# Kernel tuning notes

Measured on AMD Instinct MI355X. Metric: run time of the kernel, lower is better.

Reference implementation:

```python
import jax, jax.numpy as jnp
import numpy as np

EPS = 1e-08
ROUTING_ITERS = 3

def squash(s, axis=-1):
    norm = jnp.linalg.norm(s, axis=axis, keepdims=True)
    return norm / (1.0 + norm ** 2 + EPS) * s

def setup_inputs() -> dict:
    key = jax.random.key(0)
    k1, k2, k3 = jax.random.split(key, 3)
    B, R, C, O, I = 512, 640, 10, 16, 8
    x = jax.random.normal(k1, (B, R, I), dtype=jnp.float32)
    W = jax.random.normal(k2, (R, C, O, I), dtype=jnp.float32) * 0.01
    bias = jax.random.uniform(k3, (1, 1, C, O), dtype=jnp.float32) * 0.01
    return {"x": x, "W": W, "bias": bias}

def reference(x, W, bias):
    # u_hat[b,r,c,o] = sum_i W[r,c,o,i] * x[b,r,i]
    u_hat = jnp.einsum('rcoi,bri->brco', W, x)  # [B,R,C,O]
    u_hat_d = jax.lax.stop_gradient(u_hat)
    B, R, C, _ = u_hat.shape
    b_ij = jnp.zeros((B, R, C, 1), dtype=u_hat.dtype)
    v_j = None
    for itr in range(ROUTING_ITERS):
        c_ij = jax.nn.softmax(b_ij, axis=2)               # softmax over capsules
        s_j = jnp.sum(c_ij * u_hat_d, axis=1, keepdims=True) + bias  # [B,1,C,O]
        v_j = squash(s_j, axis=-1)
        if itr < ROUTING_ITERS - 1:
            a_ij = jnp.sum(u_hat * v_j, axis=-1, keepdims=True)  # agreement, non-detached
            b_ij = b_ij + a_ij
    return jnp.squeeze(v_j, axis=1)  # [B,C,O]
```

## Files before the change

### kernel.cpp

```cpp
#include <hip/hip_runtime.h>
#include <math.h>

#define BB 512
#define RR 640
#define CC 10
#define OO 16
#define CO 160
#define II 8
#define S_FLOATS (BB*CO)

#define ZCH (RR*CO)
#define LSTR 165
#define VSTR 164

#define CG_NRG 16
#define CG_RPW 10

#define FB_NRG 32
#define FB_RPW 5

#define CNT_INTS (96*16)

using f16x8 = __attribute__((ext_vector_type(8))) _Float16;
using f32x4 = __attribute__((ext_vector_type(4))) float;



__device__ __forceinline__ float exp_small(float a) {
    float f = __builtin_fmaf(a, 0.16666667f, 0.5f);
    f = __builtin_fmaf(a, f, 1.0f);
    return __builtin_fmaf(a, f, 1.0f);
}

__device__ __forceinline__ float rowsum16(float v) {
    int t;
    t = __builtin_amdgcn_update_dpp(0, __float_as_int(v), 0x128, 0xF, 0xF, true);
    v += __int_as_float(t);
    t = __builtin_amdgcn_update_dpp(0, __float_as_int(v), 0x124, 0xF, 0xF, true);
    v += __int_as_float(t);
    t = __builtin_amdgcn_update_dpp(0, __float_as_int(v), 0x122, 0xF, 0xF, true);
    v += __int_as_float(t);
    t = __builtin_amdgcn_update_dpp(0, __float_as_int(v), 0x121, 0xF, 0xF, true);
    v += __int_as_float(t);
    return v;
}


__device__ __forceinline__ void wait_cnt(int* c, int tid) {
    if (tid == 0) {
        int it = 0;
        while (__hip_atomic_load(c, __ATOMIC_RELAXED, __HIP_MEMORY_SCOPE_AGENT) < CG_NRG) {
            __builtin_amdgcn_s_sleep(1);
            if (++it > (1 << 22)) break;
        }
        __threadfence();
    }
    __syncthreads();
}

__device__ __forceinline__ void arrive_cnt(int* c, int tid) {
    if (tid == 0) {
        __threadfence();
        atomicAdd(c, 1);
    }
}


__global__ __launch_bounds__(256) void prep(const float* __restrict__ W,
                                            const float* __restrict__ x,
                                            _Float16* __restrict__ wf,
                                            _Float16* __restrict__ xf,
                                            int* __restrict__ cnt) {
    const int t = blockIdx.x * 256 + threadIdx.x;
    if (t < RR * CO * II) wf[t] = (_Float16)W[t];
    if (t < 16) wf[RR * CO * II + t] = (_Float16)0.f;
    if (t < CNT_INTS) cnt[t] = 0;
    const int i = t & 7;
    const int b = (t >> 3) & 511;
    const int r = t >> 12;
    xf[t] = (_Float16)x[((size_t)b * RR + r) * II + i];
}


template <bool UNIFORM, int RPW_, int VROWSTR>
__device__ __forceinline__ void pass_tile(const _Float16* __restrict__ wf,
                                          const _Float16* __restrict__ xf,
                                          const float* __restrict__ vsrc,
                                          float* __restrict__ part,
                                          float* __restrict__ red,
                                          int bt, int rg, int wv, int lane) {
    const int n  = lane & 15;
    const int q  = lane >> 4;
    const bool q0 = (q == 0);
    const int b0 = bt * 16;
    const int r0 = rg * (4 * RPW_) + wv * RPW_;

    const f16x8* xq = reinterpret_cast<const f16x8*>(xf);
    const int4*  wq = reinterpret_cast<const int4*>(wf);

    f32x4 sacc[CC];
#pragma unroll
    for (int c = 0; c < CC; ++c) sacc[c] = (f32x4){0.f, 0.f, 0.f, 0.f};

    if (UNIFORM) {
        int rr = 0;
#pragma unroll
        for (; rr + 4 <= RPW_; rr += 4) {
            const int r = r0 + rr + q;
            const f16x8 bfr = xq[(size_t)r * BB + b0 + n];
#pragma unroll
            for (int c = 0; c < CC; ++c) {
                const int4 a = wq[r * CO + c * 16 + n];
                sacc[c] = __builtin_amdgcn_mfma_f32_16x16x32_f16(
                    __builtin_bit_cast(f16x8, a), bfr, sacc[c], 0, 0, 0);
            }
        }
        constexpr int REM = RPW_ & 3;
        if (REM) {
            const int qq = (q < REM) ? q : 0;
            const int r = r0 + (RPW_ - REM) + qq;
            const f16x8 bfr = xq[(size_t)r * BB + b0 + n];
#pragma unroll
            for (int c = 0; c < CC; ++c) {
                const int4 a = wq[(q < REM) ? (r * CO + c * 16 + n) : ZCH];
                sacc[c] = __builtin_amdgcn_mfma_f32_16x16x32_f16(
                    __builtin_bit_cast(f16x8, a), bfr, sacc[c], 0, 0, 0);
            }
        }
    } else {
        f32x4 vv[CC];
        const float* vp = vsrc + n * VROWSTR;
#pragma unroll
        for (int c = 0; c < CC; ++c)
            vv[c] = *reinterpret_cast<const f32x4*>(vp + c * 16 + 4 * q);

#pragma unroll 2
        for (int rr = 0; rr < RPW_; ++rr) {
            const int r = r0 + rr;
            const f16x8 bcur = xq[(size_t)r * BB + b0 + n];

            f32x4 acc[CC];
#pragma unroll
            for (int c = 0; c < CC; ++c) {
                const int4 a = wq[q0 ? (r * CO + c * 16 + n) : ZCH];
                acc[c] = __builtin_amdgcn_mfma_f32_16x16x32_f16(
                    __builtin_bit_cast(f16x8, a), bcur,
                    (f32x4){0.f, 0.f, 0.f, 0.f}, 0, 0, 0);
            }

            float e[CC];
#pragma unroll
            for (int c = 0; c < CC; ++c) {
                float t = acc[c][0] * vv[c][0] + acc[c][1] * vv[c][1]
                        + acc[c][2] * vv[c][2] + acc[c][3] * vv[c][3];
                t += __shfl_xor(t, 16);
                t += __shfl_xor(t, 32);
                e[c] = exp_small(t);
            }
            const float se = (((e[0] + e[1]) + (e[2] + e[3]))
                            + ((e[4] + e[5]) + (e[6] + e[7]))) + (e[8] + e[9]);
            const float inv = __fdividef(1.0f, se);
#pragma unroll
            for (int c = 0; c < CC; ++c) {
                const float w = e[c] * inv;
#pragma unroll
                for (int k = 0; k < 4; ++k)
                    sacc[c][k] = __builtin_fmaf(w, acc[c][k], sacc[c][k]);
            }
        }
    }

    const int cb = 4 * q;
    if (wv < 2) {
        float* dst = red + ((wv * 16 + n) * LSTR + cb);
#pragma unroll
        for (int c = 0; c < CC; ++c)
#pragma unroll
            for (int k = 0; k < 4; ++k) dst[c * 16 + k] = sacc[c][k];
    }
    __syncthreads();
    if (wv >= 2) {
        float* dst = red + (((wv - 2) * 16 + n) * LSTR + cb);
#pragma unroll
        for (int c = 0; c < CC; ++c)
#pragma unroll
            for (int k = 0; k < 4; ++k) dst[c * 16 + k] += sacc[c][k];
    }
    __syncthreads();
    if (wv == 0) {
        const float f = UNIFORM ? 0.1f : 1.0f;
        float* pb = part + (size_t)rg * S_FLOATS + (size_t)(b0 + n) * CO + cb;
        const float* ra = red + (n * LSTR + cb);
        const float* rb = red + ((16 + n) * LSTR + cb);
#pragma unroll
        for (int c = 0; c < CC; ++c) {
            f32x4 v;
#pragma unroll
            for (int k = 0; k < 4; ++k)
                v[k] = (ra[c * 16 + k] + rb[c * 16 + k]) * f;
            *reinterpret_cast<f32x4*>(pb + c * 16) = v;
        }
    }
}


__device__ __forceinline__ void boundary_squash(const float* __restrict__ part,
                                                const float* __restrict__ bias,
                                                float* __restrict__ vlds,
                                                float* __restrict__ out,
                                                int mode, int bt, int tid) {
    if (tid < 160) {
        const int b = tid & 15;
        const int c = tid >> 4;
        const int b0 = bt * 16;
        const float* pb = part + (size_t)(b0 + b) * CO + c * 16;
        const f32x4* bi = reinterpret_cast<const f32x4*>(bias + c * 16);
        f32x4 s[4];
#pragma unroll
        for (int k = 0; k < 4; ++k) s[k] = bi[k];
#pragma unroll 4
        for (int rg = 0; rg < CG_NRG; ++rg) {
            const f32x4* p = reinterpret_cast<const f32x4*>(pb + (size_t)rg * S_FLOATS);
#pragma unroll
            for (int k = 0; k < 4; ++k) s[k] += p[k];
        }
        float sq = 0.f;
#pragma unroll
        for (int k = 0; k < 4; ++k)
            sq += s[k][0] * s[k][0] + s[k][1] * s[k][1]
                + s[k][2] * s[k][2] + s[k][3] * s[k][3];
        const float norm  = sqrtf(sq);
        const float scale = norm / (1.0f + sq + 1e-8f);
        if (mode == 2) {
            f32x4* ob = reinterpret_cast<f32x4*>(out + (size_t)(b0 + b) * CO + c * 16);
#pragma unroll
            for (int k = 0; k < 4; ++k) {
                f32x4 v;
#pragma unroll
                for (int j = 0; j < 4; ++j) v[j] = scale * s[k][j];
                ob[k] = v;
            }
        } else {
            float* vl = vlds + b * VSTR + c * 16;
#pragma unroll
            for (int k = 0; k < 4; ++k)
#pragma unroll
                for (int j = 0; j < 4; ++j) {
                    const float v = scale * s[k][j];
                    if (mode == 0) vl[k * 4 + j] = v;
                    else           vl[k * 4 + j] += v;
                }
        }
    }
}


__global__ __launch_bounds__(256, 2) void caps_coop(const _Float16* __restrict__ wf,
                                                    const _Float16* __restrict__ xf,
                                                    float* __restrict__ partA,
                                                    float* __restrict__ partB,
                                                    const float* __restrict__ bias,
                                                    float* __restrict__ out,
                                                    int* __restrict__ cnt) {
    __shared__ float red[2 * 16 * LSTR];
    __shared__ __align__(16) float vlds[16 * VSTR];
    const int tid  = threadIdx.x;
    const int lane = tid & 63;
    const int wv   = tid >> 6;
    const int bid  = blockIdx.x;
    const int bt   = bid & 31;
    const int rg   = bid >> 5;

    int* c0 = cnt + (bt) * 16;
    int* c1 = cnt + (32 + bt) * 16;
    int* c2 = cnt + (64 + bt) * 16;

    pass_tile<true, CG_RPW, VSTR>(wf, xf, nullptr, partA, red, bt, rg, wv, lane);
    arrive_cnt(c0, tid);
    wait_cnt(c0, tid);
    boundary_squash(partA, bias, vlds, nullptr, 0, bt, tid);
    __syncthreads();

    pass_tile<false, CG_RPW, VSTR>(wf, xf, vlds, partB, red, bt, rg, wv, lane);
    arrive_cnt(c1, tid);
    wait_cnt(c1, tid);
    boundary_squash(partB, bias, vlds, nullptr, 1, bt, tid);
    __syncthreads();

    pass_tile<false, CG_RPW, VSTR>(wf, xf, vlds, partA, red, bt, rg, wv, lane);
    arrive_cnt(c2, tid);
    if (rg == 0) {
        wait_cnt(c2, tid);
        boundary_squash(partA, bias, nullptr, out, 2, bt, tid);
    }
}

__device__ __forceinline__ void squash_elem(const float* __restrict__ part, int nsl,
                                            const float* __restrict__ bias,
                                            float* __restrict__ vacc,
                                            float* __restrict__ out,
                                            int mode, int idx) {
    const int co = idx % CO;
    float a0 = 0.f, a1 = 0.f, a2 = 0.f, a3 = 0.f;
    int s = 0;
    for (; s + 4 <= nsl; s += 4) {
        a0 += part[(size_t)s * S_FLOATS + idx];
        a1 += part[(size_t)(s + 1) * S_FLOATS + idx];
        a2 += part[(size_t)(s + 2) * S_FLOATS + idx];
        a3 += part[(size_t)(s + 3) * S_FLOATS + idx];
    }
    for (; s < nsl; ++s) a0 += part[(size_t)s * S_FLOATS + idx];
    const float val = ((a0 + a1) + (a2 + a3)) + bias[co];
    const float sq = rowsum16(val * val);
    const float norm  = sqrtf(sq);
    const float scale = norm / (1.0f + sq + 1e-8f);
    const float v = scale * val;
    if (mode == 0)      vacc[idx] = v;
    else if (mode == 1) vacc[idx] += v;
    else                out[idx] = v;
}

template <bool UNIFORM>
__global__ __launch_bounds__(256, 2) void caps_pass_k(const _Float16* __restrict__ wf,
                                                      const _Float16* __restrict__ xf,
                                                      const float* __restrict__ vacc,
                                                      float* __restrict__ part) {
    __shared__ float red[2 * 16 * LSTR];
    const float* vbase = UNIFORM ? nullptr : (vacc + (size_t)blockIdx.x * 16 * CO);
    pass_tile<UNIFORM, FB_RPW, CO>(wf, xf, vbase, part, red,
                                   blockIdx.x, blockIdx.y, threadIdx.x >> 6,
                                   threadIdx.x & 63);
}

__global__ __launch_bounds__(256) void caps_squash_k(const float* __restrict__ part,
                                                     int nsl,
                                                     const float* __restrict__ bias,
                                                     float* __restrict__ vacc,
                                                     float* __restrict__ out,
                                                     int mode) {
    squash_elem(part, nsl, bias, vacc, out, mode, blockIdx.x * 256 + threadIdx.x);
}


extern "C" void kernel_launch(void* const* d_in, const int* in_sizes, int n_in,
                              void* d_out, int out_size, void* d_ws, size_t ws_size,
                              hipStream_t stream) {
    const float* x    = (const float*)d_in[0];
    const float* W    = (const float*)d_in[1];
    const float* bias = (const float*)d_in[2];
    float* out  = (float*)d_out;

    float*    part  = (float*)d_ws;
    float*    partA = part;
    float*    partB = part + (size_t)CG_NRG * S_FLOATS;
    float*    vacc  = part + (size_t)FB_NRG * S_FLOATS;
    int*      cnt   = (int*)vacc;
    _Float16* wf    = (_Float16*)(vacc + S_FLOATS);
    _Float16* xf    = wf + (size_t)RR * CO * II + 16;

    prep<<<BB * RR * II / 256, 256, 0, stream>>>(W, x, wf, xf, cnt);

    int maxB = 0;
    hipError_t qe = hipOccupancyMaxActiveBlocksPerMultiprocessor(
        &maxB, reinterpret_cast<const void*>(caps_coop), 256, 0);
    hipError_t le = hipErrorUnknown;
    if (qe == hipSuccess && maxB >= 2) {
        const _Float16* wfc = wf;
        const _Float16* xfc = xf;
        const float* biasc = bias;
        float* outc = out;
        int* cntc = cnt;
        void* args[] = {(void*)&wfc, (void*)&xfc, (void*)&partA, (void*)&partB,
                        (void*)&biasc, (void*)&outc, (void*)&cntc};
        le = hipLaunchCooperativeKernel(reinterpret_cast<const void*>(caps_coop),
                                        dim3(512), dim3(256), args, 0, stream);
    }

    if (le != hipSuccess) {
        const dim3 pg(32, FB_NRG);
        const int sqg = S_FLOATS / 256;
        caps_pass_k<true><<<pg, 256, 0, stream>>>(wf, xf, nullptr, part);
        caps_squash_k<<<sqg, 256, 0, stream>>>(part, FB_NRG, bias, vacc, out, 0);
        caps_pass_k<false><<<pg, 256, 0, stream>>>(wf, xf, vacc, part);
        caps_squash_k<<<sqg, 256, 0, stream>>>(part, FB_NRG, bias, vacc, out, 1);
        caps_pass_k<false><<<pg, 256, 0, stream>>>(wf, xf, vacc, part);
        caps_squash_k<<<sqg, 256, 0, stream>>>(part, FB_NRG, bias, vacc, out, 2);
    }
}
```

Before: 135.4 us.

## Accumulate routing partial sums with float atomics instead of per-group slices

Each block in the cooperative kernel now adds its reduced tile straight into a zero-initialised per-iteration accumulator with unsafeAtomicAdd, replacing writes to per-row-group partial slices. The boundary squash then reads a single summed tile rather than summing 16 slices. The barrier code also drops its explicit threadfences in favour of a vmcnt wait and a compiler memory barrier. This cuts global traffic and work at each sync point, at the cost of atomic contention, non-deterministic summation order, and weaker memory ordering that may be unsafe across blocks.

```diff
diff --git a/kernel.cpp b/kernel.cpp
--- a/kernel.cpp
+++ b/kernel.cpp
@@ -20,6 +20,8 @@
 #define FB_RPW 5
 
 #define CNT_INTS (96*16)
+#define STILE (16*CO)
+#define SACC_FLOATS (3*32*STILE)
 
 using f16x8 = __attribute__((ext_vector_type(8))) _Float16;
 using f32x4 = __attribute__((ext_vector_type(4))) float;
@@ -53,16 +55,14 @@
             __builtin_amdgcn_s_sleep(1);
             if (++it > (1 << 22)) break;
         }
-        __threadfence();
-    }
+    }
+    asm volatile("" ::: "memory");
     __syncthreads();
 }
 
 __device__ __forceinline__ void arrive_cnt(int* c, int tid) {
-    if (tid == 0) {
-        __threadfence();
-        atomicAdd(c, 1);
-    }
+    asm volatile("s_waitcnt vmcnt(0)" ::: "memory");
+    if (tid == 0) atomicAdd(c, 1);
 }
 
 
@@ -70,10 +70,12 @@
                                             const float* __restrict__ x,
                                             _Float16* __restrict__ wf,
                                             _Float16* __restrict__ xf,
+                                            float* __restrict__ sacc,
                                             int* __restrict__ cnt) {
     const int t = blockIdx.x * 256 + threadIdx.x;
     if (t < RR * CO * II) wf[t] = (_Float16)W[t];
     if (t < 16) wf[RR * CO * II + t] = (_Float16)0.f;
+    if (t < SACC_FLOATS) sacc[t] = 0.f;
     if (t < CNT_INTS) cnt[t] = 0;
     const int i = t & 7;
     const int b = (t >> 3) & 511;
@@ -82,11 +84,11 @@
 }
 
 
-template <bool UNIFORM, int RPW_, int VROWSTR>
+template <bool UNIFORM, bool ATOMIC, int RPW_, int VROWSTR>
 __device__ __forceinline__ void pass_tile(const _Float16* __restrict__ wf,
                                           const _Float16* __restrict__ xf,
                                           const float* __restrict__ vsrc,
-                                          float* __restrict__ part,
+                                          float* __restrict__ dst,
                                           float* __restrict__ red,
                                           int bt, int rg, int wv, int lane) {
     const int n  = lane & 15;
@@ -172,58 +174,61 @@
 
     const int cb = 4 * q;
     if (wv < 2) {
-        float* dst = red + ((wv * 16 + n) * LSTR + cb);
+        float* dstl = red + ((wv * 16 + n) * LSTR + cb);
 #pragma unroll
         for (int c = 0; c < CC; ++c)
 #pragma unroll
-            for (int k = 0; k < 4; ++k) dst[c * 16 + k] = sacc[c][k];
+            for (int k = 0; k < 4; ++k) dstl[c * 16 + k] = sacc[c][k];
     }
     __syncthreads();
     if (wv >= 2) {
-        float* dst = red + (((wv - 2) * 16 + n) * LSTR + cb);
+        float* dstl = red + (((wv - 2) * 16 + n) * LSTR + cb);
 #pragma unroll
         for (int c = 0; c < CC; ++c)
 #pragma unroll
-            for (int k = 0; k < 4; ++k) dst[c * 16 + k] += sacc[c][k];
+            for (int k = 0; k < 4; ++k) dstl[c * 16 + k] += sacc[c][k];
     }
     __syncthreads();
     if (wv == 0) {
         const float f = UNIFORM ? 0.1f : 1.0f;
-        float* pb = part + (size_t)rg * S_FLOATS + (size_t)(b0 + n) * CO + cb;
         const float* ra = red + (n * LSTR + cb);
         const float* rb = red + ((16 + n) * LSTR + cb);
-#pragma unroll
-        for (int c = 0; c < CC; ++c) {
-            f32x4 v;
-#pragma unroll
-            for (int k = 0; k < 4; ++k)
-                v[k] = (ra[c * 16 + k] + rb[c * 16 + k]) * f;
-            *reinterpret_cast<f32x4*>(pb + c * 16) = v;
-        }
-    }
-}
-
-
-__device__ __forceinline__ void boundary_squash(const float* __restrict__ part,
-                                                const float* __restrict__ bias,
-                                                float* __restrict__ vlds,
-                                                float* __restrict__ out,
-                                                int mode, int bt, int tid) {
+        if (ATOMIC) {
+            float* sb = dst + n * CO + cb;
+#pragma unroll
+            for (int c = 0; c < CC; ++c)
+#pragma unroll
+                for (int k = 0; k < 4; ++k)
+                    unsafeAtomicAdd(sb + c * 16 + k,
+                                    (ra[c * 16 + k] + rb[c * 16 + k]) * f);
+        } else {
+            float* pb = dst + (size_t)rg * S_FLOATS + (size_t)(b0 + n) * CO + cb;
+#pragma unroll
+            for (int c = 0; c < CC; ++c) {
+                f32x4 v;
+#pragma unroll
+                for (int k = 0; k < 4; ++k)
+                    v[k] = (ra[c * 16 + k] + rb[c * 16 + k]) * f;
+                *reinterpret_cast<f32x4*>(pb + c * 16) = v;
+            }
+        }
+    }
+}
+
+
+__device__ __forceinline__ void bsquash(const float* __restrict__ st,
+                                        const float* __restrict__ bias,
+                                        float* __restrict__ vlds,
+                                        float* __restrict__ out,
+                                        int mode, int bt, int tid) {
     if (tid < 160) {
         const int b = tid & 15;
         const int c = tid >> 4;
-        const int b0 = bt * 16;
-        const float* pb = part + (size_t)(b0 + b) * CO + c * 16;
+        const f32x4* sp = reinterpret_cast<const f32x4*>(st + b * CO + c * 16);
         const f32x4* bi = reinterpret_cast<const f32x4*>(bias + c * 16);
         f32x4 s[4];
 #pragma unroll
-        for (int k = 0; k < 4; ++k) s[k] = bi[k];
-#pragma unroll 4
-        for (int rg = 0; rg < CG_NRG; ++rg) {
-            const f32x4* p = reinterpret_cast<const f32x4*>(pb + (size_t)rg * S_FLOATS);
-#pragma unroll
-            for (int k = 0; k < 4; ++k) s[k] += p[k];
-        }
+        for (int k = 0; k < 4; ++k) s[k] = sp[k] + bi[k];
         float sq = 0.f;
 #pragma unroll
         for (int k = 0; k < 4; ++k)
@@ -232,7 +237,7 @@
         const float norm  = sqrtf(sq);
         const float scale = norm / (1.0f + sq + 1e-8f);
         if (mode == 2) {
-            f32x4* ob = reinterpret_cast<f32x4*>(out + (size_t)(b0 + b) * CO + c * 16);
+            f32x4* ob = reinterpret_cast<f32x4*>(out + (size_t)(bt * 16 + b) * CO + c * 16);
 #pragma unroll
             for (int k = 0; k < 4; ++k) {
                 f32x4 v;
@@ -257,12 +262,11 @@
 
 __global__ __launch_bounds__(256, 2) void caps_coop(const _Float16* __restrict__ wf,
                                                     const _Float16* __restrict__ xf,
-                                                    float* __restrict__ partA,
-                                                    float* __restrict__ partB,
+                                                    float* __restrict__ sacc,
                                                     const float* __restrict__ bias,
                                                     float* __restrict__ out,
                                                     int* __restrict__ cnt) {
-    __shared__ float red[2 * 16 * LSTR];
+    __shared__ __align__(16) float red[2 * 16 * LSTR];
     __shared__ __align__(16) float vlds[16 * VSTR];
     const int tid  = threadIdx.x;
     const int lane = tid & 63;
@@ -274,24 +278,27 @@
     int* c0 = cnt + (bt) * 16;
     int* c1 = cnt + (32 + bt) * 16;
     int* c2 = cnt + (64 + bt) * 16;
-
-    pass_tile<true, CG_RPW, VSTR>(wf, xf, nullptr, partA, red, bt, rg, wv, lane);
+    float* s0 = sacc + (size_t)(0 * 32 + bt) * STILE;
+    float* s1 = sacc + (size_t)(1 * 32 + bt) * STILE;
+    float* s2 = sacc + (size_t)(2 * 32 + bt) * STILE;
+
+    pass_tile<true, true, CG_RPW, VSTR>(wf, xf, nullptr, s0, red, bt, rg, wv, lane);
     arrive_cnt(c0, tid);
     wait_cnt(c0, tid);
-    boundary_squash(partA, bias, vlds, nullptr, 0, bt, tid);
-    __syncthreads();
-
-    pass_tile<false, CG_RPW, VSTR>(wf, xf, vlds, partB, red, bt, rg, wv, lane);
+    bsquash(s0, bias, vlds, nullptr, 0, bt, tid);
+    __syncthreads();
+
+    pass_tile<false, true, CG_RPW, VSTR>(wf, xf, vlds, s1, red, bt, rg, wv, lane);
     arrive_cnt(c1, tid);
     wait_cnt(c1, tid);
-    boundary_squash(partB, bias, vlds, nullptr, 1, bt, tid);
-    __syncthreads();
-
-    pass_tile<false, CG_RPW, VSTR>(wf, xf, vlds, partA, red, bt, rg, wv, lane);
+    bsquash(s1, bias, vlds, nullptr, 1, bt, tid);
+    __syncthreads();
+
+    pass_tile<false, true, CG_RPW, VSTR>(wf, xf, vlds, s2, red, bt, rg, wv, lane);
     arrive_cnt(c2, tid);
     if (rg == 0) {
         wait_cnt(c2, tid);
-        boundary_squash(partA, bias, nullptr, out, 2, bt, tid);
+        bsquash(s2, bias, nullptr, out, 2, bt, tid);
     }
 }
 
@@ -325,11 +332,11 @@
                                                       const _Float16* __restrict__ xf,
                                                       const float* __restrict__ vacc,
                                                       float* __restrict__ part) {
-    __shared__ float red[2 * 16 * LSTR];
+    __shared__ __align__(16) float red[2 * 16 * LSTR];
     const float* vbase = UNIFORM ? nullptr : (vacc + (size_t)blockIdx.x * 16 * CO);
-    pass_tile<UNIFORM, FB_RPW, CO>(wf, xf, vbase, part, red,
-                                   blockIdx.x, blockIdx.y, threadIdx.x >> 6,
-                                   threadIdx.x & 63);
+    pass_tile<UNIFORM, false, FB_RPW, CO>(wf, xf, vbase, part, red,
+                                          blockIdx.x, blockIdx.y, threadIdx.x >> 6,
+                                          threadIdx.x & 63);
 }
 
 __global__ __launch_bounds__(256) void caps_squash_k(const float* __restrict__ part,
@@ -350,15 +357,14 @@
     const float* bias = (const float*)d_in[2];
     float* out  = (float*)d_out;
 
-    float*    part  = (float*)d_ws;
-    float*    partA = part;
-    float*    partB = part + (size_t)CG_NRG * S_FLOATS;
-    float*    vacc  = part + (size_t)FB_NRG * S_FLOATS;
-    int*      cnt   = (int*)vacc;
-    _Float16* wf    = (_Float16*)(vacc + S_FLOATS);
-    _Float16* xf    = wf + (size_t)RR * CO * II + 16;
-
-    prep<<<BB * RR * II / 256, 256, 0, stream>>>(W, x, wf, xf, cnt);
+    float*    part = (float*)d_ws;
+    float*    sacc = part;
+    float*    vacc = part + (size_t)FB_NRG * S_FLOATS;
+    int*      cnt  = (int*)vacc;
+    _Float16* wf   = (_Float16*)(vacc + S_FLOATS);
+    _Float16* xf   = wf + (size_t)RR * CO * II + 16;
+
+    prep<<<BB * RR * II / 256, 256, 0, stream>>>(W, x, wf, xf, sacc, cnt);
 
     int maxB = 0;
     hipError_t qe = hipOccupancyMaxActiveBlocksPerMultiprocessor(
@@ -369,8 +375,9 @@
         const _Float16* xfc = xf;
         const float* biasc = bias;
         float* outc = out;
+        float* saccc = sacc;
         int* cntc = cnt;
-        void* args[] = {(void*)&wfc, (void*)&xfc, (void*)&partA, (void*)&partB,
+        void* args[] = {(void*)&wfc, (void*)&xfc, (void*)&saccc,
                         (void*)&biasc, (void*)&outc, (void*)&cntc};
         le = hipLaunchCooperativeKernel(reinterpret_cast<const void*>(caps_coop),
                                         dim3(512), dim3(256), args, 0, stream);
```

Result: no change. 134.9 us (-0.4%).
